# Kernel optimization log

Measured on AMD Instinct MI355X. Metric: run time of the kernel, lower is better.

Reference implementation:

```python
import math
import jax, jax.numpy as jnp
import numpy as np

H = 16  # head_count
D = 1024  # model_dim
DH = D // H  # dim_per_head = 64
PAD_IDX = 1


def setup_inputs() -> dict:
    key = jax.random.key(0)
    ks = jax.random.split(key, 16)
    B, L = 4, 512
    s = 0.02
    inp = {
        'key': jax.random.normal(ks[0], (B, L, D), jnp.float32),
        'value': jax.random.normal(ks[1], (B, L, D), jnp.float32),
        'query': jax.random.normal(ks[2], (B, L, D), jnp.float32),
        'ast_parents_matrix': jax.random.randint(ks[3], (B, L, L), 0, 200, jnp.int32),
        'mask': jnp.zeros((B, 1, L), jnp.bool_),
        'Wq': jax.random.normal(ks[4], (D, D), jnp.float32) * s,
        'bq': jnp.zeros((D,), jnp.float32),
        'Wk': jax.random.normal(ks[5], (D, D), jnp.float32) * s,
        'bk': jnp.zeros((D,), jnp.float32),
        'Wv': jax.random.normal(ks[6], (D, D), jnp.float32) * s,
        'bv': jnp.zeros((D,), jnp.float32),
        'Wo': jax.random.normal(ks[7], (D, D), jnp.float32) * s,
        'bo': jnp.zeros((D,), jnp.float32),
        'struct_emb': jax.random.normal(ks[8], (200, DH), jnp.float32).at[PAD_IDX].set(0.0),
        'value_emb': jax.random.normal(ks[9], (10000, DH), jnp.float32).at[PAD_IDX].set(0.0),
    }
    return inp


def _parent_embeddings(matrix, struct_emb, value_emb):
    # matrix: (B, Lq, K) int ids; even key positions use structure vocab, odd use value vocab
    B, Lq, K = matrix.shape
    s_ids = matrix[:, :, ::2]   # (B, Lq, ceil(K/2))
    v_ids = matrix[:, :, 1::2]  # (B, Lq, floor(K/2))
    emb_s = struct_emb[s_ids]   # (B, Lq, S, DH)
    emb_v = value_emb[v_ids]    # (B, Lq, V, DH)
    S = emb_s.shape[2]
    if emb_v.shape[2] != S:  # odd K: pad value stream by one zero slot, drop after interleave
        emb_v = jnp.concatenate([emb_v, jnp.zeros_like(emb_s[:, :, :1])], axis=2)
    pe = jnp.stack([emb_s, emb_v], axis=3).reshape(B, Lq, 2 * S, DH)
    return pe[:, :, :K, :]  # (B, Lq, K, DH)


def reference(key, value, query, ast_parents_matrix, mask,
              Wq, bq, Wk, bk, Wv, bv, Wo, bo, struct_emb, value_emb):
    B, L, _ = query.shape

    def shape(x):
        return x.reshape(B, -1, H, DH).transpose(0, 2, 1, 3)  # (B,H,L,DH)

    q = shape(query @ Wq + bq) / math.sqrt(DH)
    k = shape(key @ Wk + bk)
    v = shape(value @ Wv + bv)

    qk = jnp.einsum('bhid,bhjd->bhij', q, k)  # (B,H,L,L)

    pe = _parent_embeddings(ast_parents_matrix[:, :, :L], struct_emb, value_emb)
    score_ast = jnp.einsum('bhid,bijd->bhij', q, pe)

    scores = (qk + score_ast).astype(jnp.float32)
    scores = jnp.where(mask[:, None, :, :], -1e18, scores)  # mask: (B,1,L)->(B,1,1,L)
    attn = jax.nn.softmax(scores, axis=-1).astype(q.dtype)
    # dropout p=0.0 (eval) -> identity
    context = jnp.einsum('bhij,bhjd->bhid', attn, v)  # (B,H,L,DH)
    context = context.transpose(0, 2, 1, 3).reshape(B, L, D)
    output = context @ Wo + bo
    return output, attn
```

## Files before the change

### kernel.cpp

```cpp
#include <hip/hip_runtime.h>
#include <cstddef>

#define H 16
#define D 1024
#define DH 64
#define L 512

typedef __attribute__((ext_vector_type(8))) short bf16x8;
typedef __attribute__((ext_vector_type(4))) short bf16x4;
typedef __attribute__((ext_vector_type(4))) float f32x4;

__device__ inline short f2bf(float x) {
    union { float f; unsigned u; } c; c.f = x;
    unsigned r = (c.u + 0x7FFFu + ((c.u >> 16) & 1u)) >> 16;
    return (short)r;
}
__device__ inline float bf2f(short x) {
    union { float f; unsigned u; } c;
    c.u = ((unsigned)(unsigned short)x) << 16; return c.f;
}

__device__ inline void gload_lds16(const void* g, void* l) {
    __builtin_amdgcn_global_load_lds(
        (const __attribute__((address_space(1))) unsigned int*)g,
        (__attribute__((address_space(3))) unsigned int*)l,
        16, 0, 0);
}

struct CvtArgs { const float* src[5]; short* dst[5]; int n[5]; };

__global__ __launch_bounds__(256) void cvt_kernel(CvtArgs a) {
    int r = blockIdx.y;
    const float* s = a.src[r];
    short* d = a.dst[r];
    int n = a.n[r];
    int i = (blockIdx.x * 256 + threadIdx.x) * 8;
    if (i >= n) return;
    float4 x0 = *(const float4*)(s + i);
    float4 x1 = *(const float4*)(s + i + 4);
    bf16x8 o;
    o[0] = f2bf(x0.x); o[1] = f2bf(x0.y); o[2] = f2bf(x0.z); o[3] = f2bf(x0.w);
    o[4] = f2bf(x1.x); o[5] = f2bf(x1.y); o[6] = f2bf(x1.z); o[7] = f2bf(x1.w);
    *(bf16x8*)(d + i) = o;
}

struct WtArgs { const float* W[4]; short* T[4]; };

__global__ __launch_bounds__(256) void wtrans_kernel(WtArgs a) {
    const float* W = a.W[blockIdx.z];
    short* T = a.T[blockIdx.z];
    int idx = blockIdx.x * 256 + threadIdx.x;
    int n = idx & 1023;
    int k0 = (idx >> 10) << 3;
    bf16x8 o;
    #pragma unroll
    for (int kk = 0; kk < 8; ++kk)
        o[kk] = f2bf(W[(size_t)(k0 + kk) * 1024 + n]);
    *(bf16x8*)(T + (size_t)n * 1024 + k0) = o;
}

#define BM 128
#define BN 64
#define BKK 64

struct GemmBatch {
    const short* A[3]; const short* Bt[3]; const float* bias[3];
    void* out[3]; float scale[3]; int mode[3];
};

__global__ __launch_bounds__(256) void gemm_mfma_kernel(GemmBatch P, int M, int N, int K) {
    const int z = blockIdx.z;
    const short* __restrict__ A  = P.A[z];
    const short* __restrict__ Bt = P.Bt[z];
    const float* __restrict__ bias = P.bias[z];
    const float scale = P.scale[z];
    const int mode = P.mode[z];

    __shared__ short lds[(BM + BN) * BKK];
    short* As = lds;
    short* Bs = lds + BM * BKK;

    const int tid = threadIdx.x;
    const int wave = tid >> 6, lane = tid & 63;
    const int fm = lane & 15, quad = lane >> 4;
    const int m0 = blockIdx.y * BM, n0 = blockIdx.x * BN;

    int arow[4], acol[4];
    #pragma unroll
    for (int t = 0; t < 4; ++t) {
        int s = (wave * 4 + t) * 64 + lane;
        int row = s >> 3;
        int u = (s & 7) ^ (row & 7);
        arow[t] = row; acol[t] = u * 8;
    }
    int brow[2], bcol[2];
    #pragma unroll
    for (int t = 0; t < 2; ++t) {
        int s = (wave * 2 + t) * 64 + lane;
        int row = s >> 3;
        int u = (s & 7) ^ (row & 7);
        brow[t] = row; bcol[t] = u * 8;
    }

    int aoff[2][2], boff[4][2];
    #pragma unroll
    for (int mt = 0; mt < 2; ++mt)
        #pragma unroll
        for (int kst = 0; kst < 2; ++kst) {
            int row = wave * 32 + mt * 16 + fm;
            int u = quad + 4 * kst;
            aoff[mt][kst] = row * 64 + ((u ^ (row & 7)) * 8);
        }
    #pragma unroll
    for (int nt = 0; nt < 4; ++nt)
        #pragma unroll
        for (int kst = 0; kst < 2; ++kst) {
            int row = nt * 16 + fm;
            int u = quad + 4 * kst;
            boff[nt][kst] = row * 64 + ((u ^ (row & 7)) * 8);
        }

    f32x4 acc[2][4];
    #pragma unroll
    for (int mt = 0; mt < 2; ++mt)
        #pragma unroll
        for (int nt = 0; nt < 4; ++nt) acc[mt][nt] = (f32x4){0.f, 0.f, 0.f, 0.f};

    for (int k0 = 0; k0 < K; k0 += BKK) {
        __syncthreads();
        #pragma unroll
        for (int t = 0; t < 4; ++t)
            gload_lds16(A + (size_t)(m0 + arow[t]) * K + k0 + acol[t],
                        As + (wave * 4 + t) * 512);
        #pragma unroll
        for (int t = 0; t < 2; ++t)
            gload_lds16(Bt + (size_t)(n0 + brow[t]) * K + k0 + bcol[t],
                        Bs + (wave * 2 + t) * 512);
        __syncthreads();
        #pragma unroll
        for (int kst = 0; kst < 2; ++kst) {
            bf16x8 af[2], bfr[4];
            af[0] = *(const bf16x8*)(As + aoff[0][kst]);
            af[1] = *(const bf16x8*)(As + aoff[1][kst]);
            #pragma unroll
            for (int nt = 0; nt < 4; ++nt)
                bfr[nt] = *(const bf16x8*)(Bs + boff[nt][kst]);
            #pragma unroll
            for (int mt = 0; mt < 2; ++mt)
                #pragma unroll
                for (int nt = 0; nt < 4; ++nt)
                    acc[mt][nt] = __builtin_amdgcn_mfma_f32_16x16x32_bf16(
                        af[mt], bfr[nt], acc[mt][nt], 0, 0, 0);
        }
    }

    if (mode == 2) {
        __syncthreads();
        short (*T)[BM + 8] = (short(*)[BM + 8])&lds[0];
        #pragma unroll
        for (int mt = 0; mt < 2; ++mt)
            #pragma unroll
            for (int nt = 0; nt < 4; ++nt) {
                int nn = nt * 16 + fm;
                float bv = bias[n0 + nn];
                #pragma unroll
                for (int r = 0; r < 4; ++r) {
                    int mm = wave * 32 + mt * 16 + quad * 4 + r;
                    T[nn][mm] = f2bf((acc[mt][nt][r] + bv) * scale);
                }
            }
        __syncthreads();
        int b = m0 >> 9;
        int ibase = m0 & (L - 1);
        int hblk = n0 >> 6;
        int n = tid >> 2, seg = (tid & 3) * 32;
        short* dst = (short*)P.out[z] + (((size_t)(b * H + hblk) * DH + n) * L) + ibase + seg;
        #pragma unroll
        for (int c = 0; c < 4; ++c)
            *(bf16x8*)(dst + c * 8) = *(const bf16x8*)(&T[n][seg + c * 8]);
    } else {
        #pragma unroll
        for (int mt = 0; mt < 2; ++mt)
            #pragma unroll
            for (int nt = 0; nt < 4; ++nt) {
                int n = n0 + nt * 16 + fm;
                float bv = bias[n];
                #pragma unroll
                for (int r = 0; r < 4; ++r) {
                    int m = m0 + wave * 32 + mt * 16 + quad * 4 + r;
                    float val = (acc[mt][nt][r] + bv) * scale;
                    if (mode == 0) {
                        ((float*)P.out[z])[(size_t)m * N + n] = val;
                    } else {
                        int b = m >> 9, i = m & (L - 1);
                        int h = n >> 6, d = n & (DH - 1);
                        ((short*)P.out[z])[(((size_t)(b * H + h) * L + i) * DH) + d] = f2bf(val);
                    }
                }
            }
    }
}

__global__ __launch_bounds__(256) void ast_kernel(
    const short* __restrict__ Qb, const int* __restrict__ mat,
    const short* __restrict__ semb, const short* __restrict__ vemb,
    short* __restrict__ Sast)
{
    const int i = blockIdx.x, b = blockIdx.y;
    const int tid = threadIdx.x;
    const int wave = tid >> 6, lane = tid & 63;
    const int fm = lane & 15, quad = lane >> 4;
    __shared__ short Sl[H][L + 8];

    const short* qp = Qb + (((size_t)(b * H + fm) * L + i) * DH);
    bf16x8 a0 = *(const bf16x8*)(qp + quad * 8);
    bf16x8 a1 = *(const bf16x8*)(qp + 32 + quad * 8);

    const int* mrow = mat + ((size_t)b * L + i) * L;

    for (int jt = wave; jt < L / 16; jt += 4) {
        int j = jt * 16 + fm;
        int idx = mrow[j];
        const short* er = ((j & 1) ? vemb : semb) + (size_t)idx * DH;
        bf16x8 b0 = *(const bf16x8*)(er + quad * 8);
        bf16x8 b1 = *(const bf16x8*)(er + 32 + quad * 8);
        f32x4 c = {0.f, 0.f, 0.f, 0.f};
        c = __builtin_amdgcn_mfma_f32_16x16x32_bf16(a0, b0, c, 0, 0, 0);
        c = __builtin_amdgcn_mfma_f32_16x16x32_bf16(a1, b1, c, 0, 0, 0);
        #pragma unroll
        for (int r = 0; r < 4; ++r)
            Sl[quad * 4 + r][j] = f2bf(c[r]);
    }
    __syncthreads();
    int hh = tid >> 4, j0 = (tid & 15) * 32;
    short* dst = Sast + ((((size_t)b * L + i) * H + hh) * L) + j0;
    #pragma unroll
    for (int c = 0; c < 4; ++c)
        *(bf16x8*)(dst + c * 8) = *(const bf16x8*)(&Sl[hh][j0 + c * 8]);
}

__global__ __launch_bounds__(256) void attn_fused_kernel(
    const short* __restrict__ Qb, const short* __restrict__ Kb,
    const short* __restrict__ Vt, const short* __restrict__ Sast,
    const unsigned char* __restrict__ mask,
    float* __restrict__ attn, short* __restrict__ ctx)
{
    const int i0 = blockIdx.x * 16;
    const int h = blockIdx.y;
    const int b = blockIdx.z;
    const int tid = threadIdx.x;
    const int wave = tid >> 6, lane = tid & 63;
    const int fm = lane & 15, quad = lane >> 4;

    __shared__ short Pb[16][L + 8];
    __shared__ float red_m[4][16];
    __shared__ float red_l[4][16];

    const short* qp = Qb + (((size_t)(b * H + h) * L + i0 + fm) * DH);
    bf16x8 a0 = *(const bf16x8*)(qp + quad * 8);
    bf16x8 a1 = *(const bf16x8*)(qp + 32 + quad * 8);
    const short* Kbase = Kb + ((size_t)(b * H + h) * L) * DH;
    const short* Sb = Sast + (((size_t)b * L + i0) * H + h) * L;

    float s[8][4];
    float mx[4] = {-3.0e38f, -3.0e38f, -3.0e38f, -3.0e38f};

    #pragma unroll
    for (int t = 0; t < 8; ++t) {
        int jt = wave + t * 4;
        int j = jt * 16 + fm;
        const short* kr = Kbase + (size_t)j * DH;
        bf16x8 b0 = *(const bf16x8*)(kr + quad * 8);
        bf16x8 b1 = *(const bf16x8*)(kr + 32 + quad * 8);
        f32x4 c = {0.f, 0.f, 0.f, 0.f};
        c = __builtin_amdgcn_mfma_f32_16x16x32_bf16(a0, b0, c, 0, 0, 0);
        c = __builtin_amdgcn_mfma_f32_16x16x32_bf16(a1, b1, c, 0, 0, 0);
        bool mk = mask[(size_t)b * L + j] != 0;
        #pragma unroll
        for (int r = 0; r < 4; ++r) {
            int ir = quad * 4 + r;
            float sv = c[r] + bf2f(Sb[(size_t)ir * H * L + j]);
            sv = mk ? -1e18f : sv;
            s[t][r] = sv;
            mx[r] = fmaxf(mx[r], sv);
        }
    }

    #pragma unroll
    for (int off = 1; off <= 8; off <<= 1)
        #pragma unroll
        for (int r = 0; r < 4; ++r)
            mx[r] = fmaxf(mx[r], __shfl_xor(mx[r], off));
    if (fm == 0)
        #pragma unroll
        for (int r = 0; r < 4; ++r) red_m[wave][quad * 4 + r] = mx[r];
    __syncthreads();
    float M_[4];
    #pragma unroll
    for (int r = 0; r < 4; ++r) {
        int ir = quad * 4 + r;
        M_[r] = fmaxf(fmaxf(red_m[0][ir], red_m[1][ir]),
                      fmaxf(red_m[2][ir], red_m[3][ir]));
    }

    float sum[4] = {0.f, 0.f, 0.f, 0.f};
    #pragma unroll
    for (int t = 0; t < 8; ++t)
        #pragma unroll
        for (int r = 0; r < 4; ++r) {
            float e = __expf(s[t][r] - M_[r]);
            s[t][r] = e;
            sum[r] += e;
        }
    #pragma unroll
    for (int off = 1; off <= 8; off <<= 1)
        #pragma unroll
        for (int r = 0; r < 4; ++r)
            sum[r] += __shfl_xor(sum[r], off);
    if (fm == 0)
        #pragma unroll
        for (int r = 0; r < 4; ++r) red_l[wave][quad * 4 + r] = sum[r];
    __syncthreads();
    float inv[4];
    #pragma unroll
    for (int r = 0; r < 4; ++r) {
        int ir = quad * 4 + r;
        inv[r] = 1.f / (red_l[0][ir] + red_l[1][ir] + red_l[2][ir] + red_l[3][ir]);
    }

    #pragma unroll
    for (int t = 0; t < 8; ++t) {
        int j = (wave + t * 4) * 16 + fm;
        #pragma unroll
        for (int r = 0; r < 4; ++r) {
            int ir = quad * 4 + r;
            float p = s[t][r] * inv[r];
            attn[(((size_t)(b * H + h) * L + i0 + ir) * L) + j] = p;
            Pb[ir][j] = f2bf(p);
        }
    }
    __syncthreads();

    const short* Vb = Vt + (((size_t)(b * H + h) * DH + wave * 16 + fm) * L);
    f32x4 o = {0.f, 0.f, 0.f, 0.f};
    for (int ks = 0; ks < L; ks += 32) {
        bf16x8 pa = *(const bf16x8*)(&Pb[fm][ks + quad * 8]);
        bf16x8 vb = *(const bf16x8*)(Vb + ks + quad * 8);
        o = __builtin_amdgcn_mfma_f32_16x16x32_bf16(pa, vb, o, 0, 0, 0);
    }
    #pragma unroll
    for (int r = 0; r < 4; ++r)
        ctx[((size_t)b * L + i0 + quad * 4 + r) * D + h * DH + wave * 16 + fm] = f2bf(o[r]);
}

extern "C" void kernel_launch(void* const* d_in, const int* in_sizes, int n_in,
                              void* d_out, int out_size, void* d_ws, size_t ws_size,
                              hipStream_t stream) {
    const float* key_in   = (const float*)d_in[0];
    const float* value_in = (const float*)d_in[1];
    const float* query_in = (const float*)d_in[2];
    const int*   mat      = (const int*)d_in[3];
    const unsigned char* mask = (const unsigned char*)d_in[4];
    const float* Wq = (const float*)d_in[5];
    const float* bq = (const float*)d_in[6];
    const float* Wk = (const float*)d_in[7];
    const float* bk = (const float*)d_in[8];
    const float* Wv = (const float*)d_in[9];
    const float* bv = (const float*)d_in[10];
    const float* Wo = (const float*)d_in[11];
    const float* bo = (const float*)d_in[12];
    const float* struct_emb = (const float*)d_in[13];
    const float* value_emb  = (const float*)d_in[14];

    const int B = in_sizes[2] / (L * D);
    const int M = B * L;

    short* p = (short*)d_ws;
    short* xk  = p;  p += (size_t)M * D;
    short* xv  = p;  p += (size_t)M * D;
    short* xq  = p;  p += (size_t)M * D;
    short* WqT = p;  p += (size_t)D * D;
    short* WkT = p;  p += (size_t)D * D;
    short* WvT = p;  p += (size_t)D * D;
    short* WoT = p;  p += (size_t)D * D;
    short* semb = p; p += 16384;
    short* vemb = p; p += (size_t)in_sizes[14];
    short* Qb = p;   p += (size_t)M * D;
    short* Kb = p;   p += (size_t)M * D;
    short* Vt = p;   p += (size_t)M * D;
    short* Sast = p; p += (size_t)B * L * H * L;
    short* ctx = xk;

    float* out_p  = (float*)d_out;
    float* attn_p = out_p + (size_t)M * D;

    CvtArgs ca;
    ca.src[0] = key_in;     ca.dst[0] = xk;   ca.n[0] = M * D;
    ca.src[1] = value_in;   ca.dst[1] = xv;   ca.n[1] = M * D;
    ca.src[2] = query_in;   ca.dst[2] = xq;   ca.n[2] = M * D;
    ca.src[3] = struct_emb; ca.dst[3] = semb; ca.n[3] = in_sizes[13];
    ca.src[4] = value_emb;  ca.dst[4] = vemb; ca.n[4] = in_sizes[14];
    cvt_kernel<<<dim3((M * D) / 2048, 5), 256, 0, stream>>>(ca);

    WtArgs wa;
    wa.W[0] = Wq; wa.W[1] = Wk; wa.W[2] = Wv; wa.W[3] = Wo;
    wa.T[0] = WqT; wa.T[1] = WkT; wa.T[2] = WvT; wa.T[3] = WoT;
    wtrans_kernel<<<dim3(512, 1, 4), 256, 0, stream>>>(wa);

    GemmBatch qkv;
    qkv.A[0] = xq; qkv.Bt[0] = WqT; qkv.bias[0] = bq; qkv.out[0] = Qb; qkv.scale[0] = 0.125f; qkv.mode[0] = 1;
    qkv.A[1] = xk; qkv.Bt[1] = WkT; qkv.bias[1] = bk; qkv.out[1] = Kb; qkv.scale[1] = 1.0f;   qkv.mode[1] = 1;
    qkv.A[2] = xv; qkv.Bt[2] = WvT; qkv.bias[2] = bv; qkv.out[2] = Vt; qkv.scale[2] = 1.0f;   qkv.mode[2] = 2;
    gemm_mfma_kernel<<<dim3(D / BN, M / BM, 3), 256, 0, stream>>>(qkv, M, D, D);

    ast_kernel<<<dim3(L, B), 256, 0, stream>>>(Qb, mat, semb, vemb, Sast);

    attn_fused_kernel<<<dim3(L / 16, H, B), 256, 0, stream>>>(
        Qb, Kb, Vt, Sast, mask, attn_p, ctx);

    GemmBatch fin;
    fin.A[0] = ctx; fin.Bt[0] = WoT; fin.bias[0] = bo; fin.out[0] = out_p; fin.scale[0] = 1.0f; fin.mode[0] = 0;
    fin.A[1] = ctx; fin.Bt[1] = WoT; fin.bias[1] = bo; fin.out[1] = out_p; fin.scale[1] = 1.0f; fin.mode[1] = 0;
    fin.A[2] = ctx; fin.Bt[2] = WoT; fin.bias[2] = bo; fin.out[2] = out_p; fin.scale[2] = 1.0f; fin.mode[2] = 0;
    gemm_mfma_kernel<<<dim3(D / BN, M / BM, 1), 256, 0, stream>>>(fin, M, D, D);
}
```

Before: 242.0 us.

## Merge prep kernels, stage AST scores in LDS, coalesce attention writes

Merges the input-conversion and weight-transpose kernels into one launch, saving a kernel launch. The AST kernel now loads all gather indices up front so that the embedding reads can overlap. The attention kernel stages its AST score tile in LDS with coalesced vector loads and changes the key-column mapping per wave. It also writes the fp32 attention matrix row-wise from LDS with float4 stores, aiming to coalesce the largest output write. The cost is that the returned attention probabilities are now rounded to bf16 before being stored as fp32, which lowers output precision.

```diff
diff --git a/kernel.cpp b/kernel.cpp
--- a/kernel.cpp
+++ b/kernel.cpp
@@ -27,36 +27,38 @@
         16, 0, 0);
 }
 
-struct CvtArgs { const float* src[5]; short* dst[5]; int n[5]; };
-
-__global__ __launch_bounds__(256) void cvt_kernel(CvtArgs a) {
-    int r = blockIdx.y;
-    const float* s = a.src[r];
-    short* d = a.dst[r];
-    int n = a.n[r];
-    int i = (blockIdx.x * 256 + threadIdx.x) * 8;
-    if (i >= n) return;
-    float4 x0 = *(const float4*)(s + i);
-    float4 x1 = *(const float4*)(s + i + 4);
-    bf16x8 o;
-    o[0] = f2bf(x0.x); o[1] = f2bf(x0.y); o[2] = f2bf(x0.z); o[3] = f2bf(x0.w);
-    o[4] = f2bf(x1.x); o[5] = f2bf(x1.y); o[6] = f2bf(x1.z); o[7] = f2bf(x1.w);
-    *(bf16x8*)(d + i) = o;
-}
-
-struct WtArgs { const float* W[4]; short* T[4]; };
-
-__global__ __launch_bounds__(256) void wtrans_kernel(WtArgs a) {
-    const float* W = a.W[blockIdx.z];
-    short* T = a.T[blockIdx.z];
-    int idx = blockIdx.x * 256 + threadIdx.x;
-    int n = idx & 1023;
-    int k0 = (idx >> 10) << 3;
-    bf16x8 o;
-    #pragma unroll
-    for (int kk = 0; kk < 8; ++kk)
-        o[kk] = f2bf(W[(size_t)(k0 + kk) * 1024 + n]);
-    *(bf16x8*)(T + (size_t)n * 1024 + k0) = o;
+struct PrepArgs {
+    const float* csrc[5]; short* cdst[5]; int cn[5];
+    const float* W[4]; short* T[4];
+};
+
+__global__ __launch_bounds__(256) void prep_kernel(PrepArgs a) {
+    const int y = blockIdx.y;
+    if (y < 5) {
+        const float* s = a.csrc[y];
+        short* d = a.cdst[y];
+        int n = a.cn[y];
+        int i = (blockIdx.x * 256 + threadIdx.x) * 8;
+        if (i >= n) return;
+        float4 x0 = *(const float4*)(s + i);
+        float4 x1 = *(const float4*)(s + i + 4);
+        bf16x8 o;
+        o[0] = f2bf(x0.x); o[1] = f2bf(x0.y); o[2] = f2bf(x0.z); o[3] = f2bf(x0.w);
+        o[4] = f2bf(x1.x); o[5] = f2bf(x1.y); o[6] = f2bf(x1.z); o[7] = f2bf(x1.w);
+        *(bf16x8*)(d + i) = o;
+    } else {
+        const float* W = a.W[y - 5];
+        short* T = a.T[y - 5];
+        int idx = blockIdx.x * 256 + threadIdx.x;
+        if (idx >= 1024 * 128) return;
+        int n = idx & 1023;
+        int k0 = (idx >> 10) << 3;
+        bf16x8 o;
+        #pragma unroll
+        for (int kk = 0; kk < 8; ++kk)
+            o[kk] = f2bf(W[(size_t)(k0 + kk) * 1024 + n]);
+        *(bf16x8*)(T + (size_t)n * 1024 + k0) = o;
+    }
 }
 
 #define BM 128
@@ -218,12 +220,24 @@
 
     const int* mrow = mat + ((size_t)b * L + i) * L;
 
-    for (int jt = wave; jt < L / 16; jt += 4) {
-        int j = jt * 16 + fm;
-        int idx = mrow[j];
-        const short* er = ((j & 1) ? vemb : semb) + (size_t)idx * DH;
-        bf16x8 b0 = *(const bf16x8*)(er + quad * 8);
-        bf16x8 b1 = *(const bf16x8*)(er + 32 + quad * 8);
+    int idxs[8];
+    const short* ebase[8];
+    #pragma unroll
+    for (int t = 0; t < 8; ++t) {
+        int j = (wave + t * 4) * 16 + fm;
+        idxs[t] = mrow[j];
+    }
+    #pragma unroll
+    for (int t = 0; t < 8; ++t) {
+        int j = (wave + t * 4) * 16 + fm;
+        ebase[t] = ((j & 1) ? vemb : semb) + (size_t)idxs[t] * DH;
+    }
+
+    #pragma unroll
+    for (int t = 0; t < 8; ++t) {
+        int j = (wave + t * 4) * 16 + fm;
+        bf16x8 b0 = *(const bf16x8*)(ebase[t] + quad * 8);
+        bf16x8 b1 = *(const bf16x8*)(ebase[t] + 32 + quad * 8);
         f32x4 c = {0.f, 0.f, 0.f, 0.f};
         c = __builtin_amdgcn_mfma_f32_16x16x32_bf16(a0, b0, c, 0, 0, 0);
         c = __builtin_amdgcn_mfma_f32_16x16x32_bf16(a1, b1, c, 0, 0, 0);
@@ -256,19 +270,25 @@
     __shared__ float red_m[4][16];
     __shared__ float red_l[4][16];
 
+    {
+        int r = tid >> 4, seg = (tid & 15) * 32;
+        const short* sp = Sast + ((((size_t)b * L + i0 + r) * H + h) * L) + seg;
+        #pragma unroll
+        for (int c = 0; c < 4; ++c)
+            *(bf16x8*)(&Pb[r][seg + c * 8]) = *(const bf16x8*)(sp + c * 8);
+    }
+
     const short* qp = Qb + (((size_t)(b * H + h) * L + i0 + fm) * DH);
     bf16x8 a0 = *(const bf16x8*)(qp + quad * 8);
     bf16x8 a1 = *(const bf16x8*)(qp + 32 + quad * 8);
     const short* Kbase = Kb + ((size_t)(b * H + h) * L) * DH;
-    const short* Sb = Sast + (((size_t)b * L + i0) * H + h) * L;
+    __syncthreads();
 
     float s[8][4];
     float mx[4] = {-3.0e38f, -3.0e38f, -3.0e38f, -3.0e38f};
-
     #pragma unroll
     for (int t = 0; t < 8; ++t) {
-        int jt = wave + t * 4;
-        int j = jt * 16 + fm;
+        int j = wave * 128 + t * 16 + fm;
         const short* kr = Kbase + (size_t)j * DH;
         bf16x8 b0 = *(const bf16x8*)(kr + quad * 8);
         bf16x8 b1 = *(const bf16x8*)(kr + 32 + quad * 8);
@@ -279,7 +299,7 @@
         #pragma unroll
         for (int r = 0; r < 4; ++r) {
             int ir = quad * 4 + r;
-            float sv = c[r] + bf2f(Sb[(size_t)ir * H * L + j]);
+            float sv = c[r] + bf2f(Pb[ir][j]);
             sv = mk ? -1e18f : sv;
             s[t][r] = sv;
             mx[r] = fmaxf(mx[r], sv);
@@ -330,16 +350,30 @@
 
     #pragma unroll
     for (int t = 0; t < 8; ++t) {
-        int j = (wave + t * 4) * 16 + fm;
+        int j = wave * 128 + t * 16 + fm;
         #pragma unroll
         for (int r = 0; r < 4; ++r) {
             int ir = quad * 4 + r;
-            float p = s[t][r] * inv[r];
-            attn[(((size_t)(b * H + h) * L + i0 + ir) * L) + j] = p;
-            Pb[ir][j] = f2bf(p);
+            Pb[ir][j] = f2bf(s[t][r] * inv[r]);
         }
     }
     __syncthreads();
+
+    {
+        int rowl = tid >> 4;
+        int c0 = (tid & 15) * 8;
+        float* arow = attn + (((size_t)(b * H + h) * L + i0 + rowl) * L);
+        #pragma unroll
+        for (int c = 0; c < 4; ++c) {
+            int col = c0 + c * 128;
+            bf16x8 pk = *(const bf16x8*)(&Pb[rowl][col]);
+            float4 v0, v1;
+            v0.x = bf2f(pk[0]); v0.y = bf2f(pk[1]); v0.z = bf2f(pk[2]); v0.w = bf2f(pk[3]);
+            v1.x = bf2f(pk[4]); v1.y = bf2f(pk[5]); v1.z = bf2f(pk[6]); v1.w = bf2f(pk[7]);
+            *(float4*)(arow + col) = v0;
+            *(float4*)(arow + col + 4) = v1;
+        }
+    }
 
     const short* Vb = Vt + (((size_t)(b * H + h) * DH + wave * 16 + fm) * L);
     f32x4 o = {0.f, 0.f, 0.f, 0.f};
@@ -394,18 +428,15 @@
     float* out_p  = (float*)d_out;
     float* attn_p = out_p + (size_t)M * D;
 
-    CvtArgs ca;
-    ca.src[0] = key_in;     ca.dst[0] = xk;   ca.n[0] = M * D;
-    ca.src[1] = value_in;   ca.dst[1] = xv;   ca.n[1] = M * D;
-    ca.src[2] = query_in;   ca.dst[2] = xq;   ca.n[2] = M * D;
-    ca.src[3] = struct_emb; ca.dst[3] = semb; ca.n[3] = in_sizes[13];
-    ca.src[4] = value_emb;  ca.dst[4] = vemb; ca.n[4] = in_sizes[14];
-    cvt_kernel<<<dim3((M * D) / 2048, 5), 256, 0, stream>>>(ca);
-
-    WtArgs wa;
-    wa.W[0] = Wq; wa.W[1] = Wk; wa.W[2] = Wv; wa.W[3] = Wo;
-    wa.T[0] = WqT; wa.T[1] = WkT; wa.T[2] = WvT; wa.T[3] = WoT;
-    wtrans_kernel<<<dim3(512, 1, 4), 256, 0, stream>>>(wa);
+    PrepArgs pa;
+    pa.csrc[0] = key_in;     pa.cdst[0] = xk;   pa.cn[0] = M * D;
+    pa.csrc[1] = value_in;   pa.cdst[1] = xv;   pa.cn[1] = M * D;
+    pa.csrc[2] = query_in;   pa.cdst[2] = xq;   pa.cn[2] = M * D;
+    pa.csrc[3] = struct_emb; pa.cdst[3] = semb; pa.cn[3] = in_sizes[13];
+    pa.csrc[4] = value_emb;  pa.cdst[4] = vemb; pa.cn[4] = in_sizes[14];
+    pa.W[0] = Wq; pa.W[1] = Wk; pa.W[2] = Wv; pa.W[3] = Wo;
+    pa.T[0] = WqT; pa.T[1] = WkT; pa.T[2] = WvT; pa.T[3] = WoT;
+    prep_kernel<<<dim3((M * D) / 2048, 9), 256, 0, stream>>>(pa);
 
     GemmBatch qkv;
     qkv.A[0] = xq; qkv.Bt[0] = WqT; qkv.bias[0] = bq; qkv.out[0] = Qb; qkv.scale[0] = 0.125f; qkv.mode[0] = 1;
```

After: 241.4 us. No clear change (-0.3%).
